# Kernel optimization log

Measured on AMD Instinct MI355X. Metric: run time of the kernel, lower is better.

The kernel has to match this reference:

```python
import jax, jax.numpy as jnp
import numpy as np


def setup_inputs() -> dict:
    B, S, D, V = 2, 4096, 512, 32000
    FE_START, FE_LEN = 5, 3062          # user-controllable span [5, 3067)
    ADV_START, ADV_LEN = 1000, 64       # adversarial suffix block
    ML = ADV_START - FE_START           # 995 = max_left_shift
    MR = FE_LEN - (ADV_START - FE_START + ADV_LEN)  # 2003 = max_right_shift
    key = jax.random.key(0)
    k1, k2 = jax.random.split(key)
    input_ids = jax.random.randint(k1, (B, S), 0, V, dtype=jnp.int32)
    suffix_mask = jnp.zeros((B, S), dtype=bool).at[:, ADV_START:ADV_START + ADV_LEN].set(True)
    # param initialized like _create_parameters: delta at index max_left_shift
    param = jnp.zeros((1, ML + MR + 1), dtype=jnp.float32).at[0, ML].set(1.0)
    emb_weight = jax.random.normal(k2, (V, D), dtype=jnp.float32) * 0.02
    return {
        'input_ids': input_ids, 'suffix_mask': suffix_mask,
        'param': param, 'emb_weight': emb_weight,
        'fe_start': FE_START, 'fe_len': FE_LEN, 'adv_len': ADV_LEN,
        'max_left_shift': ML, 'max_right_shift': MR,
    }


def _padded_kernel(param, ml, mr):
    left_pad = max(0, mr - ml)
    right_pad = max(0, ml - mr)
    # F.pad then flip, as in torch forward
    return jnp.flip(jnp.pad(param, ((0, 0), (left_pad, right_pad)))[0])  # (Kp,)


def reference(input_ids, suffix_mask, param, emb_weight,
              fe_start, fe_len, adv_len, max_left_shift, max_right_shift):
    B, S = input_ids.shape
    D = emb_weight.shape[1]
    Kp = 2 * max(max_left_shift, max_right_shift) + 1
    p = Kp // 2  # 'same' padding
    pk = _padded_kernel(param, max_left_shift, max_right_shift).astype(emb_weight.dtype)

    embeds = emb_weight[input_ids]                       # (B,S,D)
    fe = embeds[:, fe_start:fe_start + fe_len]           # frontend-user gather (contiguous)
    fe_pad = jnp.pad(fe, ((0, 0), (p, p), (0, 0)))       # (B, F+2p, D)
    # depthwise conv1d with a single shared kernel == Toeplitz matmul
    off = jnp.arange(fe_len + 2 * p)[None, :] - jnp.arange(fe_len)[:, None]
    W = jnp.where((off >= 0) & (off < Kp), pk[jnp.clip(off, 0, Kp - 1)], 0.0)  # (F, F+2p)
    new_fe = jnp.einsum('tu,bud->btd', W, fe_pad)        # (B,F,D)
    # scatter-concat: other[:extra0] | shifted user span | other[extra1:]
    out_embeds = jnp.concatenate(
        [embeds[:, :fe_start], new_fe, embeds[:, fe_start + fe_len:]], axis=1)

    # ----- id path (no_grad in original) -----
    L = adv_len
    ms = p - jnp.argmax(pk == 1.0)                       # mask_shift
    a0 = jnp.argmax(suffix_mask, axis=-1)                # (B,) current_start
    ns = a0 + ms                                         # new_start
    idx = jnp.arange(S - L)[None, :]
    src = idx + L * (idx >= a0[:, None])                 # skip the adv block
    nonadv = jnp.take_along_axis(input_ids, src, axis=1)             # (B,S-L)
    adv = jnp.take_along_axis(input_ids, a0[:, None] + jnp.arange(L)[None, :], axis=1)
    j = jnp.arange(S)[None, :]
    in_adv = (j >= ns[:, None]) & (j < ns[:, None] + L)
    idx_non = jnp.clip(jnp.where(j < ns[:, None], j, j - L), 0, S - L - 1)
    idx_adv = jnp.clip(j - ns[:, None], 0, L - 1)
    out_ids = jnp.where(in_adv,
                        jnp.take_along_axis(adv, idx_adv, axis=1),
                        jnp.take_along_axis(nonadv, idx_non, axis=1))
    return out_embeds, out_ids
```

## Files before the change

### kernel.cpp

```cpp
#include <hip/hip_runtime.h>
#include <limits.h>

#define BB 2
#define SS 4096
#define DD 512
#define VV 32000
#define FE_START 5
#define FE_LEN 3062
#define ADV_LEN 64
#define ML 995
#define MR 2003
#define KP (2 * MR + 1)
#define PHALF (KP / 2)
#define LEFT_PAD (MR - ML)
#define PARAM_LEN (ML + MR + 1)

typedef float floatx4 __attribute__((ext_vector_type(4)));



__global__ void ABS_meta_kernel(const unsigned char* __restrict__ mask_bytes,
                                const float* __restrict__ param,
                                int* __restrict__ meta,
                                int tap_cap) {
    __shared__ int s_nnz;
    __shared__ int s_jmax;
    __shared__ int s_firstb;
    __shared__ int s_layout;
    __shared__ int s_off0;
    __shared__ float s_w0;
    __shared__ int s_a0b[BB];
    __shared__ int s_a0i[BB];

    const int tid = threadIdx.x;
    const int nt = blockDim.x;
    if (tid == 0) {
        s_nnz = 0; s_jmax = -1; s_firstb = INT_MAX;
        s_off0 = INT_MAX; s_w0 = 0.0f;
    }
    if (tid < BB) { s_a0b[tid] = INT_MAX; s_a0i[tid] = INT_MAX; }
    __syncthreads();

    const unsigned long long* m8 = (const unsigned long long*)mask_bytes;
    for (int i = tid; i < (BB * SS) / 8; i += nt) {
        unsigned long long w = m8[i];
        if (w) {
            int fb = i * 8 + (__ffsll((long long)w) - 1) / 8;
            atomicMin(&s_firstb, fb);
            #pragma unroll
            for (int k = 0; k < 8; ++k) {
                if ((w >> (8 * k)) & 0xffull) {
                    int pos = i * 8 + k;
                    atomicMin(&s_a0b[pos / SS], pos % SS);
                }
            }
            if ((unsigned int)w) {
                int pos = 2 * i;
                atomicMin(&s_a0i[pos / SS], pos % SS);
            }
            if ((unsigned int)(w >> 32)) {
                int pos = 2 * i + 1;
                atomicMin(&s_a0i[pos / SS], pos % SS);
            }
        }
    }

    for (int j = tid; j < PARAM_LEN; j += nt) {
        float w = param[j];
        if (w != 0.0f) {
            int slot = atomicAdd(&s_nnz, 1);
            if (slot < tap_cap) {
                int* tp = meta + 16 + 2 * slot;
                tp[0] = 995 - j;
                ((float*)tp)[1] = w;
            }
            if (slot == 0) { s_off0 = 995 - j; s_w0 = w; }
        }
        if (w == 1.0f) atomicMax(&s_jmax, j);
    }
    __syncthreads();

    if (tid == 0) {
        int f = s_firstb;
        int layout = 1;
        if (f != INT_MAX) {
            layout = (f + 1 < BB * SS && mask_bytes[f + 1] != 0) ? 1 : 4;
        }
        s_layout = layout;
    }
    __syncthreads();

    if (s_layout == 4) {
        for (int i = (BB * SS) / 8 + tid; i < (4 * BB * SS) / 8; i += nt) {
            unsigned long long w = m8[i];
            if (w) {
                if ((unsigned int)w) {
                    int pos = 2 * i;
                    atomicMin(&s_a0i[pos / SS], pos % SS);
                }
                if ((unsigned int)(w >> 32)) {
                    int pos = 2 * i + 1;
                    atomicMin(&s_a0i[pos / SS], pos % SS);
                }
            }
        }
        __syncthreads();
    }

    if (tid == 0) {
        meta[0] = (s_nnz < tap_cap) ? s_nnz : tap_cap;
        meta[1] = (s_jmax >= 0) ? (s_jmax - 995) : PHALF;
        for (int b = 0; b < BB; ++b) {
            int a0 = (s_layout == 1) ? s_a0b[b] : s_a0i[b];
            meta[2 + b] = (a0 == INT_MAX) ? 0 : a0;
        }
        meta[4] = (s_nnz == 1 && s_off0 == 0 && s_w0 == 1.0f) ? 1 : 0;
    }
}

__global__ void __launch_bounds__(128)
ABS_embed_ids_kernel(const int* __restrict__ ids,
                     const float* __restrict__ emb,
                     const int* __restrict__ meta,
                     float* __restrict__ out) {
    const int bt = blockIdx.x;
    const int b = bt / SS;
    const int t = bt % SS;
    const int d4 = threadIdx.x;

    floatx4* out4 = (floatx4*)(out + (size_t)bt * DD);
    floatx4 res;

    const bool in_fe = (t >= FE_START) && (t < FE_START + FE_LEN);
    bool copy_path = !in_fe;
    if (in_fe && meta[4]) copy_path = true;

    if (copy_path) {
        const int id = ids[bt];
        res = ((const floatx4*)(emb + (size_t)id * DD))[d4];
    } else {
        const int tt = t - FE_START;
        const int nnz = meta[0];
        floatx4 acc = (floatx4)(0.f);
        for (int k = 0; k < nnz; ++k) {
            const int* tp = meta + 16 + 2 * k;
            const int off = tp[0];
            const float w = ((const float*)tp)[1];
            const int s = tt + off;
            if (s >= 0 && s < FE_LEN) {
                const int id = ids[b * SS + FE_START + s];
                const floatx4 v = ((const floatx4*)(emb + (size_t)id * DD))[d4];
                acc += w * v;
            }
        }
        res = acc;
    }

    __builtin_nontemporal_store(res, &out4[d4]);

    if (threadIdx.x == 0) {
        const int ms = meta[1];
        const int a0 = meta[2 + b];
        const int ns = a0 + ms;
        const int j = t;
        int outid;
        if (j >= ns && j < ns + ADV_LEN) {
            outid = ids[b * SS + a0 + (j - ns)];
        } else {
            int k = (j < ns) ? j : (j - ADV_LEN);
            k = min(max(k, 0), SS - ADV_LEN - 1);
            const int src = k + ((k >= a0) ? ADV_LEN : 0);
            outid = ids[b * SS + src];
        }
        __builtin_nontemporal_store((float)outid,
                                    out + (size_t)BB * SS * DD + bt);
    }
}

extern "C" void kernel_launch(void* const* d_in, const int* in_sizes, int n_in,
                              void* d_out, int out_size, void* d_ws, size_t ws_size,
                              hipStream_t stream) {
    const int* ids = (const int*)d_in[0];
    const unsigned char* mask = (const unsigned char*)d_in[1];
    const float* param = (const float*)d_in[2];
    const float* emb = (const float*)d_in[3];
    float* out = (float*)d_out;
    int* meta = (int*)d_ws;

    int tap_cap = (int)((ws_size > 128 ? ws_size - 64 : 64) / 8);
    if (tap_cap > KP) tap_cap = KP;

    ABS_meta_kernel<<<1, 1024, 0, stream>>>(mask, param, meta, tap_cap);
    ABS_embed_ids_kernel<<<BB * SS, 128, 0, stream>>>(ids, emb, meta, out);
}
```

Before: 123.1 us.

## Fuse metadata scan into embedding kernel and process four rows per block

Drops the single-block metadata kernel. Every block of the gather kernel now rescans the param vector and its own batch's mask to derive taps, shift and adversarial start in shared memory. Each block handles four rows with 256 threads, two float4s per thread. This removes one launch and the serialized 1-block prologue, but repeats the roughly 3K-element param scan and the mask scan in all 2048 blocks.

Measured after the change: 122.5 us. No clear change (-0.5%).

```diff
diff --git a/kernel.cpp b/kernel.cpp
--- a/kernel.cpp
+++ b/kernel.cpp
@@ -12,168 +12,149 @@
 #define MR 2003
 #define KP (2 * MR + 1)
 #define PHALF (KP / 2)
-#define LEFT_PAD (MR - ML)
 #define PARAM_LEN (ML + MR + 1)
+
+#define ROWS 4
+#define TPB 256
+#define TAP_CAP 128
 
 typedef float floatx4 __attribute__((ext_vector_type(4)));
 
-
-
-__global__ void ABS_meta_kernel(const unsigned char* __restrict__ mask_bytes,
-                                const float* __restrict__ param,
-                                int* __restrict__ meta,
-                                int tap_cap) {
+__global__ void __launch_bounds__(TPB)
+ABS_fused_kernel(const int* __restrict__ ids,
+                 const unsigned char* __restrict__ mask_bytes,
+                 const float* __restrict__ param,
+                 const float* __restrict__ emb,
+                 float* __restrict__ out) {
     __shared__ int s_nnz;
     __shared__ int s_jmax;
-    __shared__ int s_firstb;
+    __shared__ int s_a0b;
+    __shared__ int s_a0i;
     __shared__ int s_layout;
-    __shared__ int s_off0;
-    __shared__ float s_w0;
-    __shared__ int s_a0b[BB];
-    __shared__ int s_a0i[BB];
+    __shared__ int s_toff[TAP_CAP];
+    __shared__ float s_tw[TAP_CAP];
 
     const int tid = threadIdx.x;
-    const int nt = blockDim.x;
-    if (tid == 0) {
-        s_nnz = 0; s_jmax = -1; s_firstb = INT_MAX;
-        s_off0 = INT_MAX; s_w0 = 0.0f;
-    }
-    if (tid < BB) { s_a0b[tid] = INT_MAX; s_a0i[tid] = INT_MAX; }
+    const int blocks_per_b = SS / ROWS;
+    const int b = blockIdx.x / blocks_per_b;
+    const int t0 = (blockIdx.x % blocks_per_b) * ROWS;
+
+    if (tid == 0) { s_nnz = 0; s_jmax = -1; s_a0b = INT_MAX; s_a0i = INT_MAX; }
     __syncthreads();
 
-    const unsigned long long* m8 = (const unsigned long long*)mask_bytes;
-    for (int i = tid; i < (BB * SS) / 8; i += nt) {
-        unsigned long long w = m8[i];
-        if (w) {
-            int fb = i * 8 + (__ffsll((long long)w) - 1) / 8;
-            atomicMin(&s_firstb, fb);
-            #pragma unroll
-            for (int k = 0; k < 8; ++k) {
-                if ((w >> (8 * k)) & 0xffull) {
-                    int pos = i * 8 + k;
-                    atomicMin(&s_a0b[pos / SS], pos % SS);
-                }
-            }
-            if ((unsigned int)w) {
-                int pos = 2 * i;
-                atomicMin(&s_a0i[pos / SS], pos % SS);
-            }
-            if ((unsigned int)(w >> 32)) {
-                int pos = 2 * i + 1;
-                atomicMin(&s_a0i[pos / SS], pos % SS);
-            }
+    for (int j = tid; j < PARAM_LEN; j += TPB) {
+        const float w = param[j];
+        if (w != 0.0f) {
+            const int slot = atomicAdd(&s_nnz, 1);
+            if (slot < TAP_CAP) { s_toff[slot] = 995 - j; s_tw[slot] = w; }
         }
+        if (w == 1.0f) atomicMax(&s_jmax, j);
     }
 
-    for (int j = tid; j < PARAM_LEN; j += nt) {
-        float w = param[j];
-        if (w != 0.0f) {
-            int slot = atomicAdd(&s_nnz, 1);
-            if (slot < tap_cap) {
-                int* tp = meta + 16 + 2 * slot;
-                tp[0] = 995 - j;
-                ((float*)tp)[1] = w;
-            }
-            if (slot == 0) { s_off0 = 995 - j; s_w0 = w; }
+    const unsigned long long* m8 = (const unsigned long long*)mask_bytes;
+    for (int i = tid; i < SS / 8; i += TPB) {
+        const unsigned long long w = m8[(size_t)b * (SS / 8) + i];
+        if (w) {
+            const int byteidx = i * 8 + (__ffsll((long long)w) - 1) / 8;
+            atomicMin(&s_a0b, byteidx);
         }
-        if (w == 1.0f) atomicMax(&s_jmax, j);
     }
     __syncthreads();
 
     if (tid == 0) {
-        int f = s_firstb;
-        int layout = 1;
-        if (f != INT_MAX) {
-            layout = (f + 1 < BB * SS && mask_bytes[f + 1] != 0) ? 1 : 4;
+        int layout;
+        if (s_a0b == INT_MAX) {
+            layout = 4;
+        } else {
+            const int fb = b * SS + s_a0b;
+            layout = (mask_bytes[fb + 1] != 0) ? 1 : 4;
         }
         s_layout = layout;
     }
     __syncthreads();
 
     if (s_layout == 4) {
-        for (int i = (BB * SS) / 8 + tid; i < (4 * BB * SS) / 8; i += nt) {
-            unsigned long long w = m8[i];
+        for (int i = tid; i < SS / 2; i += TPB) {
+            const unsigned long long w = m8[(size_t)b * (SS / 2) + i];
             if (w) {
-                if ((unsigned int)w) {
-                    int pos = 2 * i;
-                    atomicMin(&s_a0i[pos / SS], pos % SS);
-                }
-                if ((unsigned int)(w >> 32)) {
-                    int pos = 2 * i + 1;
-                    atomicMin(&s_a0i[pos / SS], pos % SS);
-                }
+                if ((unsigned int)w)         atomicMin(&s_a0i, 2 * i);
+                if ((unsigned int)(w >> 32)) atomicMin(&s_a0i, 2 * i + 1);
             }
         }
         __syncthreads();
     }
 
-    if (tid == 0) {
-        meta[0] = (s_nnz < tap_cap) ? s_nnz : tap_cap;
-        meta[1] = (s_jmax >= 0) ? (s_jmax - 995) : PHALF;
-        for (int b = 0; b < BB; ++b) {
-            int a0 = (s_layout == 1) ? s_a0b[b] : s_a0i[b];
-            meta[2 + b] = (a0 == INT_MAX) ? 0 : a0;
+    const int nnz = s_nnz;
+    const int ms = (s_jmax >= 0) ? (s_jmax - 995) : PHALF;
+    int a0 = (s_layout == 1) ? s_a0b : s_a0i;
+    if (a0 == INT_MAX) a0 = 0;
+    const bool ident = (nnz == 1) && (s_toff[0] == 0) && (s_tw[0] == 1.0f);
+
+    const int row = tid >> 6;
+    const int lane = tid & 63;
+    const int t = t0 + row;
+    const int bt = b * SS + t;
+    const int f4a = 2 * lane, f4b = 2 * lane + 1;
+
+    floatx4 ra, rb;
+    const bool in_fe = (t >= FE_START) && (t < FE_START + FE_LEN);
+
+    if (!in_fe || ident) {
+        const int id = ids[bt];
+        const floatx4* src = (const floatx4*)(emb + (size_t)id * DD);
+        ra = src[f4a];
+        rb = src[f4b];
+    } else {
+        const int tt = t - FE_START;
+        floatx4 aa = (floatx4)(0.f), ab = (floatx4)(0.f);
+        if (nnz <= TAP_CAP) {
+            for (int k = 0; k < nnz; ++k) {
+                const int s = tt + s_toff[k];
+                const float w = s_tw[k];
+                if (s >= 0 && s < FE_LEN) {
+                    const int id = ids[b * SS + FE_START + s];
+                    const floatx4* src = (const floatx4*)(emb + (size_t)id * DD);
+                    aa += w * src[f4a];
+                    ab += w * src[f4b];
+                }
+            }
+        } else {
+            for (int j = 0; j < PARAM_LEN; ++j) {
+                const float w = param[j];
+                if (w != 0.0f) {
+                    const int s = tt + (995 - j);
+                    if (s >= 0 && s < FE_LEN) {
+                        const int id = ids[b * SS + FE_START + s];
+                        const floatx4* src = (const floatx4*)(emb + (size_t)id * DD);
+                        aa += w * src[f4a];
+                        ab += w * src[f4b];
+                    }
+                }
+            }
         }
-        meta[4] = (s_nnz == 1 && s_off0 == 0 && s_w0 == 1.0f) ? 1 : 0;
+        ra = aa;
+        rb = ab;
     }
-}
-
-__global__ void __launch_bounds__(128)
-ABS_embed_ids_kernel(const int* __restrict__ ids,
-                     const float* __restrict__ emb,
-                     const int* __restrict__ meta,
-                     float* __restrict__ out) {
-    const int bt = blockIdx.x;
-    const int b = bt / SS;
-    const int t = bt % SS;
-    const int d4 = threadIdx.x;
 
     floatx4* out4 = (floatx4*)(out + (size_t)bt * DD);
-    floatx4 res;
+    __builtin_nontemporal_store(ra, &out4[f4a]);
+    __builtin_nontemporal_store(rb, &out4[f4b]);
 
-    const bool in_fe = (t >= FE_START) && (t < FE_START + FE_LEN);
-    bool copy_path = !in_fe;
-    if (in_fe && meta[4]) copy_path = true;
-
-    if (copy_path) {
-        const int id = ids[bt];
-        res = ((const floatx4*)(emb + (size_t)id * DD))[d4];
-    } else {
-        const int tt = t - FE_START;
-        const int nnz = meta[0];
-        floatx4 acc = (floatx4)(0.f);
-        for (int k = 0; k < nnz; ++k) {
-            const int* tp = meta + 16 + 2 * k;
-            const int off = tp[0];
-            const float w = ((const float*)tp)[1];
-            const int s = tt + off;
-            if (s >= 0 && s < FE_LEN) {
-                const int id = ids[b * SS + FE_START + s];
-                const floatx4 v = ((const floatx4*)(emb + (size_t)id * DD))[d4];
-                acc += w * v;
-            }
-        }
-        res = acc;
-    }
-
-    __builtin_nontemporal_store(res, &out4[d4]);
-
-    if (threadIdx.x == 0) {
-        const int ms = meta[1];
-        const int a0 = meta[2 + b];
+    if (tid < ROWS) {
+        const int tj = t0 + tid;
+        const int btj = b * SS + tj;
         const int ns = a0 + ms;
-        const int j = t;
         int outid;
-        if (j >= ns && j < ns + ADV_LEN) {
-            outid = ids[b * SS + a0 + (j - ns)];
+        if (tj >= ns && tj < ns + ADV_LEN) {
+            outid = ids[b * SS + a0 + (tj - ns)];
         } else {
-            int k = (j < ns) ? j : (j - ADV_LEN);
+            int k = (tj < ns) ? tj : (tj - ADV_LEN);
             k = min(max(k, 0), SS - ADV_LEN - 1);
             const int src = k + ((k >= a0) ? ADV_LEN : 0);
             outid = ids[b * SS + src];
         }
         __builtin_nontemporal_store((float)outid,
-                                    out + (size_t)BB * SS * DD + bt);
+                                    out + (size_t)BB * SS * DD + btj);
     }
 }
 
@@ -185,11 +166,8 @@
     const float* param = (const float*)d_in[2];
     const float* emb = (const float*)d_in[3];
     float* out = (float*)d_out;
-    int* meta = (int*)d_ws;
+    (void)d_ws; (void)ws_size;
 
-    int tap_cap = (int)((ws_size > 128 ? ws_size - 64 : 64) / 8);
-    if (tap_cap > KP) tap_cap = KP;
-
-    ABS_meta_kernel<<<1, 1024, 0, stream>>>(mask, param, meta, tap_cap);
-    ABS_embed_ids_kernel<<<BB * SS, 128, 0, stream>>>(ids, emb, meta, out);
+    ABS_fused_kernel<<<BB * (SS / ROWS), TPB, 0, stream>>>(ids, mask, param,
+                                                           emb, out);
 }
```
